# Optimization experiments

Hardware: AMD Instinct MI355X
Metric: run time of the kernel (lower is better)

## Reference

```python
import jax, jax.numpy as jnp
import numpy as np

B, S = 512, 256
NUM_LOC, NUM_USERS, D = 50000, 10000, 256
MAX_RECENT = 5
DQ = D // 4            # user/hour/weekday embed dim
TEMP = 3 * DQ          # temporal feature size
H2 = D // 2            # scorer hidden
NEG = -1e9


def setup_inputs() -> dict:
    key = jax.random.key(0)
    ks = jax.random.split(key, 25)
    p = lambda i, shape: jax.random.normal(ks[i], shape, jnp.float32) * 0.02

    locations = jax.random.randint(ks[0], (B, S), 0, NUM_LOC)
    users = jax.random.randint(ks[1], (B, S), 0, NUM_USERS)
    weekdays = jax.random.randint(ks[2], (B, S), 0, 8)
    start_mins = jax.random.randint(ks[3], (B, S), 0, 1440)
    lengths = jax.random.randint(ks[4], (B,), 1, S + 1)  # ragged valid lengths
    mask = jnp.arange(S)[None, :] < lengths[:, None]     # (B,S) bool prefix mask

    return {
        "locations": locations, "users": users, "weekdays": weekdays,
        "start_mins": start_mins, "mask": mask,
        # embedding tables (padding_idx=0 row zeroed, matching torch init)
        "loc_table": p(5, (NUM_LOC, D)).at[0].set(0.0),
        "user_table": p(6, (NUM_USERS, DQ)).at[0].set(0.0),
        "hour_table": p(7, (25, DQ)).at[0].set(0.0),
        "wd_table": p(8, (8, DQ)).at[0].set(0.0),
        # LSTM (PyTorch layout: gates i,f,g,o stacked)
        "W_ih": p(9, (4 * D, D + TEMP)), "W_hh": p(10, (4 * D, D)),
        "b_ih": p(11, (4 * D,)), "b_hh": p(12, (4 * D,)),
        # recent-location scorer MLP
        "sc_W1": p(13, (H2, D + 2)), "sc_b1": p(14, (H2,)),
        "sc_W2": p(15, (1, H2)), "sc_b2": p(16, (1,)),
        # new-location predictor MLP (dropout is identity in eval)
        "np_W1": p(17, (D, D)), "np_b1": p(18, (D,)),
        "np_W2": p(19, (NUM_LOC, D)), "np_b2": p(20, (NUM_LOC,)),
        # mix predictor
        "mx_W": p(21, (1, D)), "mx_b": p(22, (1,)),
    }


def _forward(locations, users, weekdays, start_mins, mask,
             loc_table, user_table, hour_table, wd_table,
             W_ih, W_hh, b_ih, b_hh,
             sc_W1, sc_b1, sc_W2, sc_b2,
             np_W1, np_b1, np_W2, np_b2, mx_W, mx_b):
    gelu = lambda x: jax.nn.gelu(x, approximate=False)  # torch nn.GELU default

    hours = jnp.clip(start_mins // 60, 0, 24)
    temporal = jnp.concatenate(
        [user_table[users], hour_table[hours], wd_table[weekdays]], axis=-1)
    x = jnp.concatenate([loc_table[locations], temporal], axis=-1)  # (B,S,D+TEMP)

    # --- LSTM over time via scan (PyTorch gate order i,f,g,o) ---
    def step(carry, xt):
        h, c = carry
        g = xt @ W_ih.T + b_ih + h @ W_hh.T + b_hh
        i, f, gg, o = jnp.split(g, 4, axis=-1)
        c = jax.nn.sigmoid(f) * c + jax.nn.sigmoid(i) * jnp.tanh(gg)
        h = jax.nn.sigmoid(o) * jnp.tanh(c)
        return (h, c), h

    h0 = jnp.zeros((x.shape[0], D), x.dtype)
    _, outs = jax.lax.scan(step, (h0, h0), jnp.swapaxes(x, 0, 1))
    output = jnp.swapaxes(outs, 0, 1)  # (B,S,D)

    seq_lens = mask.sum(axis=1).astype(jnp.int32) - 1  # last valid index
    bids = jnp.arange(output.shape[0])
    context = output[bids, seq_lens]                   # (B,D)

    # --- vectorized ragged recent-location scoring (j=0 is last visit) ---
    j = jnp.arange(MAX_RECENT)
    idx = seq_lens[:, None] - j[None, :]               # (B,R) indices from end
    valid = idx >= 0                                   # j < seq_len_b
    idxc = jnp.clip(idx, 0, S - 1)
    bidx = bids[:, None]
    rlocs = locations[bidx, idxc]                      # (B,R)
    rtimes = start_mins[bidx, idxc]
    cur_time = start_mins[bids, seq_lens][:, None]
    tdiff = ((cur_time - rtimes).astype(jnp.float32) / 1440.0)[..., None]
    pos = jnp.broadcast_to(j.astype(jnp.float32), rlocs.shape)[..., None]
    feats = jnp.concatenate([loc_table[rlocs], tdiff, pos], axis=-1)  # (B,R,D+2)
    scores = (gelu(feats @ sc_W1.T + sc_b1) @ sc_W2.T + sc_b2)[..., 0]  # (B,R)

    # drop entry jj if some newer valid entry j' < jj has the same location.
    eq = rlocs[:, :, None] == rlocs[:, None, :]        # (B, jj, j')
    newer = (j[:, None] > j[None, :])[None]            # jj > j'
    dup = jnp.any(eq & newer & valid[:, None, :], axis=-1)
    keep = valid & ~dup
    scatter_locs = jnp.where(keep, rlocs, NUM_LOC)     # out-of-range -> dropped

    recent_logits = jnp.full((rlocs.shape[0], NUM_LOC), NEG, jnp.float32)
    recent_logits = recent_logits.at[bidx, scatter_locs].set(scores, mode='drop')

    new_logits = gelu(context @ np_W1.T + np_b1) @ np_W2.T + np_b2  # (B,NUM_LOC)
    mix = jax.nn.sigmoid(context @ mx_W.T + mx_b) * 0.9 + 0.05     # (B,1)
    return mix * recent_logits + (1.0 - mix) * new_logits


def reference(locations, users, weekdays, start_mins, mask,
              loc_table, user_table, hour_table, wd_table,
              W_ih, W_hh, b_ih, b_hh,
              sc_W1, sc_b1, sc_W2, sc_b2,
              np_W1, np_b1, np_W2, np_b2, mx_W, mx_b):
    return _forward(locations, users, weekdays, start_mins, mask,
                    loc_table, user_table, hour_table, wd_table,
                    W_ih, W_hh, b_ih, b_hh,
                    sc_W1, sc_b1, sc_W2, sc_b2,
                    np_W1, np_b1, np_W2, np_b2, mx_W, mx_b)
```

## Files before the change

### kernel.cpp

```cpp
#include <hip/hip_runtime.h>
#include <hip/hip_bf16.h>
#include <math.h>

#define B_ 512
#define S_ 256
#define D_ 256
#define NLOC 50000
#define KX 448
#define G4 1024
#define NEGV -1000000000.0f

typedef __attribute__((ext_vector_type(8))) short short8;
typedef __attribute__((ext_vector_type(4))) float f32x4;

__device__ __forceinline__ float sigmoidf_(float x){ return 1.0f/(1.0f+expf(-x)); }
__device__ __forceinline__ float geluf_(float x){ return 0.5f*x*(1.0f+erff(x*0.70710678118654752f)); }
__device__ __forceinline__ unsigned short f2bf_(float x){
  __hip_bfloat16 h = __float2bfloat16(x);
  return *(unsigned short*)&h;
}
__device__ __forceinline__ float bf2f_(unsigned short u){
  __hip_bfloat16 h = *(__hip_bfloat16*)&u;
  return __bfloat162float(h);
}
__device__ __forceinline__ float fsig_(float x){
  return __fdividef(1.0f, 1.0f + __expf(-x));
}
__device__ __forceinline__ float ftanh2_(float x){
  float ax = fabsf(x);
  float x2 = x*x;
  float tp = x*(1.0f + x2*(-0.3333333333f + x2*(0.1333333333f + x2*(-0.05396825397f))));
  float e  = __expf(2.0f*fminf(ax, 15.0f));
  float te = 1.0f - __fdividef(2.0f, e + 1.0f);
  te = copysignf(te, x);
  return ax < 0.25f ? tp : te;
}
__device__ __forceinline__ void gld_lds16_(const unsigned short* gsrc, unsigned short* ldst){
  __builtin_amdgcn_global_load_lds((const __attribute__((address_space(1))) void*)gsrc,
                                   (__attribute__((address_space(3))) void*)ldst, 16, 0, 0);
}

__global__ void k_init(int* flag){
  if (blockIdx.x==0 && threadIdx.x==0) *flag = 0;
}

__global__ void k_detect(const unsigned char* m, int* flag){
  int i = blockIdx.x*256 + threadIdx.x;
  if ((i & 1) && i < B_*S_ && m[i]) atomicOr(flag, 1);
}

__global__ void k_seqlen(const void* mp, const int* flag, int* slens){
  int b = blockIdx.x*256 + threadIdx.x;
  if (b >= B_) return;
  int cnt = 0;
  if (*flag){
    const unsigned char* m = (const unsigned char*)mp;
    for (int s=0;s<S_;s++) cnt += (m[b*S_+s] != 0);
  } else {
    const int* m = (const int*)mp;
    for (int s=0;s<S_;s++) cnt += (m[b*S_+s] != 0);
  }
  slens[b] = cnt - 1;
}

__global__ void k_buildw(const float* wih, const float* bih, const float* bhh,
                         unsigned short* Wihbf, float* btot){
  int i = blockIdx.x*256 + threadIdx.x;
  if (i < G4*KX) Wihbf[i] = f2bf_(wih[i]);
  if (i < G4) btot[i] = bih[i] + bhh[i];
}

__global__ void k_packw(const float* __restrict__ whh, unsigned short* __restrict__ Whw){
  int idx = blockIdx.x*256 + threadIdx.x;
  if (idx >= 32768) return;
  int lane = idx & 63, f = (idx>>6)&7, kt = (idx>>9)&7, w = idx>>12;
  int q = f>>1, nt = f&1, l16 = lane&15, quad = lane>>4;
  int row = q*256 + w*32 + nt*16 + l16;
  int col = kt*32 + quad*8;
  const float* s = whh + (size_t)row*256 + col;
  short8 pk;
  #pragma unroll
  for (int e=0;e<8;e++) pk[e] = f2bf_(s[e]);
  *(short8*)(Whw + (size_t)idx*8) = pk;
}

__global__ __launch_bounds__(256) void k_gx(
    const int* __restrict__ loc, const int* __restrict__ usr,
    const int* __restrict__ wdy, const int* __restrict__ sm,
    const float* __restrict__ loct, const float* __restrict__ usert,
    const float* __restrict__ hourt, const float* __restrict__ wdt,
    const unsigned short* __restrict__ Wihbf, const float* __restrict__ btot,
    unsigned short* __restrict__ Gx){
  __shared__ unsigned short As[128][40];
  int tid = threadIdx.x;
  int n0 = blockIdx.x*128, m0 = blockIdx.y*128;
  int w = tid>>6, lane = tid&63;
  int quad = lane>>4, l16 = lane&15;
  int mw = (w>>1)*64, nw = (w&1)*64;
  f32x4 acc[4][4] = {};
  int r0 = tid>>2, seg = tid&3;
  for (int kt=0; kt<14; kt++){
    int k0 = kt*32;
    int kc = k0 + seg*8;
    #pragma unroll
    for (int rr=0; rr<2; rr++){
      int r = r0 + rr*64;
      int row = m0 + r;
      const float* src;
      if (kc < 256)      src = loct  + (size_t)loc[row]*256 + kc;
      else if (kc < 320) src = usert + (size_t)usr[row]*64 + (kc-256);
      else if (kc < 384) { int s = sm[row]; int hh = s/60; if (hh>24) hh=24; if (hh<0) hh=0;
                           src = hourt + (size_t)hh*64 + (kc-320); }
      else               src = wdt   + (size_t)wdy[row]*64 + (kc-384);
      float4 v0 = *(const float4*)(src);
      float4 v1 = *(const float4*)(src+4);
      short8 pk;
      pk[0]=f2bf_(v0.x); pk[1]=f2bf_(v0.y); pk[2]=f2bf_(v0.z); pk[3]=f2bf_(v0.w);
      pk[4]=f2bf_(v1.x); pk[5]=f2bf_(v1.y); pk[6]=f2bf_(v1.z); pk[7]=f2bf_(v1.w);
      *(short8*)&As[r][seg*8] = pk;
    }
    __syncthreads();
    short8 bfrag[4], afrag[4];
    #pragma unroll
    for (int nt=0; nt<4; nt++)
      bfrag[nt] = *(const short8*)(Wihbf + (size_t)(n0+nw+nt*16+l16)*KX + k0 + quad*8);
    #pragma unroll
    for (int mt=0; mt<4; mt++)
      afrag[mt] = *(const short8*)&As[mw+mt*16+l16][quad*8];
    #pragma unroll
    for (int mt=0; mt<4; mt++)
      #pragma unroll
      for (int nt=0; nt<4; nt++)
        acc[mt][nt] = __builtin_amdgcn_mfma_f32_16x16x32_bf16(afrag[mt], bfrag[nt], acc[mt][nt], 0, 0, 0);
    __syncthreads();
  }
  #pragma unroll
  for (int nt=0; nt<4; nt++){
    int col = n0 + nw + nt*16 + l16;
    float bv = btot[col];
    #pragma unroll
    for (int mt=0; mt<4; mt++){
      #pragma unroll
      for (int i=0; i<4; i++){
        int row = m0 + mw + mt*16 + quad*4 + i;
        int bb = row >> 8, tt = row & 255;
        Gx[((size_t)tt*B_ + bb)*G4 + col] = f2bf_(acc[mt][nt][i] + bv);
      }
    }
  }
}

__global__ __launch_bounds__(512, 2) void k_lstm(
    const unsigned short* __restrict__ Gx,
    const unsigned short* __restrict__ Whw,
    float* __restrict__ ctx, const int* __restrict__ slens){
  __shared__ unsigned short h_s[16][256];
  __shared__ unsigned short gx_s[16*1024];
  __shared__ unsigned short whhl[8][8][512];
  __shared__ unsigned short whr[8][4][512];
  int tid = threadIdx.x;
  int w = tid >> 6, lane = tid & 63;
  int quad = lane >> 4, l16 = lane & 15;
  int b0 = blockIdx.x * 16;
  int dw = w * 32;

  for (int i = tid; i < 16*256; i += 512) ((unsigned short*)h_s)[i] = 0;

  #pragma unroll
  for (int c=0; c<8; c++)
    gld_lds16_(Whw + ((size_t)(w*64 + c))*512 + lane*8, &whhl[w][c][0]);

  float cst[2][4] = {{0.f,0.f,0.f,0.f},{0.f,0.f,0.f,0.f}};
  int slq[4];
  #pragma unroll
  for (int i=0;i<4;i++) slq[i] = slens[b0 + quad*4 + i];

  asm volatile("s_waitcnt vmcnt(0) lgkmcnt(0)" ::: "memory");
  __syncthreads();

  const unsigned short* sb = Whw + ((size_t)(w*64 + 8))*512 + lane*8;

  for (int t=0; t<S_; t++){
    {
      const unsigned short* src = Gx + ((size_t)t*B_ + b0)*G4 + w*2048 + lane*8;
      #pragma unroll
      for (int j=0;j<4;j++) gld_lds16_(src + j*512, &gx_s[w*2048 + j*512]);
    }
    #pragma unroll
    for (int j=0;j<3;j++) gld_lds16_(sb + (size_t)j*512, &whr[w][j][0]);
    __builtin_amdgcn_sched_barrier(0);

    short8 af[8];
    #pragma unroll
    for (int kt=0;kt<8;kt++)
      af[kt] = *(const short8*)((const char*)h_s + l16*512 + ((((kt<<2)|quad) ^ (l16&7))<<4));
    f32x4 acc[4][2] = {};
    #pragma unroll
    for (int f=0;f<8;f++)
      acc[f>>1][f&1] = __builtin_amdgcn_mfma_f32_16x16x32_bf16(
          af[0], *(const short8*)&whhl[w][f][lane*8], acc[f>>1][f&1], 0, 0, 0);
    __builtin_amdgcn_sched_barrier(0);

    #pragma unroll
    for (int i=0;i<56;i++){
      if (i+3 < 56) gld_lds16_(sb + (size_t)(i+3)*512, &whr[w][(i+3)&3][0]);
      if (i <= 52)      asm volatile("s_waitcnt vmcnt(3)" ::: "memory");
      else if (i == 53) asm volatile("s_waitcnt vmcnt(2)" ::: "memory");
      else if (i == 54) asm volatile("s_waitcnt vmcnt(1)" ::: "memory");
      else              asm volatile("s_waitcnt vmcnt(0)" ::: "memory");
      __builtin_amdgcn_sched_barrier(0);
      short8 bb = *(const short8*)&whr[w][i&3][lane*8];
      int c = 8+i;
      acc[(c&7)>>1][c&1] = __builtin_amdgcn_mfma_f32_16x16x32_bf16(
          af[c>>3], bb, acc[(c&7)>>1][c&1], 0, 0, 0);
    }

    asm volatile("s_waitcnt vmcnt(0) lgkmcnt(0)" ::: "memory");
    __builtin_amdgcn_sched_barrier(0);
    __builtin_amdgcn_s_barrier();

    const unsigned int* gxw = (const unsigned int*)&gx_s[0];
    int half = l16 & 1;
    #pragma unroll
    for (int nt=0;nt<2;nt++){
      int d = dw + nt*16 + l16;
      int dbase2 = (dw + nt*16) >> 1;
      int chunkx = d >> 3;
      #pragma unroll
      for (int i=0;i<4;i++){
        int r = quad*4 + i;
        int base = r*512 + dbase2 + (l16>>1);
        unsigned int u0 = gxw[base];
        unsigned int u1 = gxw[base + 128];
        unsigned int u2 = gxw[base + 256];
        unsigned int u3 = gxw[base + 384];
        unsigned short s0 = half ? (unsigned short)(u0>>16) : (unsigned short)(u0&0xffff);
        unsigned short s1 = half ? (unsigned short)(u1>>16) : (unsigned short)(u1&0xffff);
        unsigned short s2 = half ? (unsigned short)(u2>>16) : (unsigned short)(u2&0xffff);
        unsigned short s3 = half ? (unsigned short)(u3>>16) : (unsigned short)(u3&0xffff);
        float gi = acc[0][nt][i] + bf2f_(s0);
        float gf = acc[1][nt][i] + bf2f_(s1);
        float gg = acc[2][nt][i] + bf2f_(s2);
        float go = acc[3][nt][i] + bf2f_(s3);
        float cn = fsig_(gf)*cst[nt][i] + fsig_(gi)*ftanh2_(gg);
        float hn = fsig_(go)*ftanh2_(cn);
        cst[nt][i] = cn;
        *(unsigned short*)((char*)h_s + r*512 + ((chunkx ^ (r&7))<<4) + (d&7)*2) = f2bf_(hn);
        if (t == slq[i]) ctx[(size_t)(b0 + r)*D_ + d] = hn;
      }
    }

    asm volatile("s_waitcnt lgkmcnt(0)" ::: "memory");
    __builtin_amdgcn_sched_barrier(0);
    __builtin_amdgcn_s_barrier();
  }
}

__global__ void k_post1(const float* __restrict__ ctx, const float* __restrict__ W1,
                        const float* __restrict__ b1, const float* __restrict__ mxW,
                        const float* __restrict__ mxb, float* newhid, float* mixv){
  __shared__ float cs[256];
  __shared__ float red[256];
  int b = blockIdx.x, tid = threadIdx.x;
  cs[tid] = ctx[(size_t)b*D_ + tid];
  __syncthreads();
  float a = b1[tid];
  const float* wr = W1 + (size_t)tid*D_;
  for (int k=0; k<D_; k++) a += cs[k]*wr[k];
  newhid[(size_t)b*D_ + tid] = geluf_(a);
  red[tid] = cs[tid]*mxW[tid];
  __syncthreads();
  for (int s=128; s>0; s>>=1){ if (tid<s) red[tid]+=red[tid+s]; __syncthreads(); }
  if (tid==0) mixv[b] = sigmoidf_(red[0]+mxb[0])*0.9f + 0.05f;
}

__global__ void k_recent(const int* __restrict__ loc, const int* __restrict__ sm,
                         const int* __restrict__ slens, const float* __restrict__ loct,
                         const float* __restrict__ W1, const float* __restrict__ b1,
                         const float* __restrict__ W2, const float* __restrict__ b2,
                         float* scores, int* rlocs, int* keep){
  __shared__ int rl[5], vs[5];
  __shared__ float td[5];
  __shared__ float red[128];
  int b = blockIdx.x, tid = threadIdx.x;
  int sl = slens[b];
  if (tid < 5){
    int idx = sl - tid;
    int v = idx >= 0;
    int ic = v ? idx : 0;
    rl[tid] = loc[b*S_ + ic];
    vs[tid] = v;
    int cur = sm[b*S_ + sl];
    td[tid] = (float)(cur - sm[b*S_ + ic]) * (1.0f/1440.0f);
  }
  __syncthreads();
  for (int j=0; j<5; j++){
    const float* lrow = loct + (size_t)rl[j]*D_;
    const float* wr = W1 + (size_t)tid*258;
    float a = b1[tid];
    for (int k=0; k<D_; k++) a += lrow[k]*wr[k];
    a += td[j]*wr[256] + (float)j*wr[257];
    red[tid] = geluf_(a)*W2[tid];
    __syncthreads();
    for (int s=64; s>0; s>>=1){ if (tid<s) red[tid]+=red[tid+s]; __syncthreads(); }
    if (tid==0) scores[b*5+j] = red[0] + b2[0];
    __syncthreads();
  }
  if (tid==0){
    for (int j=0; j<5; j++){
      int dup = 0;
      for (int k=0; k<j; k++) dup |= (rl[j]==rl[k]) && vs[k];
      keep[b*5+j] = vs[j] && !dup;
      rlocs[b*5+j] = rl[j];
    }
  }
}

__global__ __launch_bounds__(256) void k_final(const float* __restrict__ newhid,
    const float* __restrict__ W2, const float* __restrict__ b2,
    const float* __restrict__ mixv, float* __restrict__ out){
  __shared__ float Hs[16][260];
  __shared__ float Wl[64][65];
  int tid = threadIdx.x;
  int l0 = blockIdx.x*64, b0 = blockIdx.y*16;
  int ll = tid & 63, bq = tid >> 6;
  #pragma unroll
  for (int r=0; r<16; r++) Hs[r][tid] = newhid[(size_t)(b0+r)*D_ + tid];
  float acc[4] = {0.f,0.f,0.f,0.f};
  for (int kt=0; kt<4; kt++){
    int k0 = kt*64;
    __syncthreads();
    #pragma unroll
    for (int r=0; r<4; r++){
      int row = 4*r + bq;
      int l = l0 + row;
      Wl[row][ll] = (l < NLOC) ? W2[(size_t)l*D_ + k0 + ll] : 0.f;
    }
    __syncthreads();
    #pragma unroll
    for (int kk=0; kk<64; kk++){
      float wv = Wl[ll][kk];
      #pragma unroll
      for (int bi=0; bi<4; bi++) acc[bi] += wv * Hs[bq*4+bi][k0+kk];
    }
  }
  int l = l0 + ll;
  if (l < NLOC){
    float bias = b2[l];
    #pragma unroll
    for (int bi=0; bi<4; bi++){
      int b = b0 + bq*4 + bi;
      float mx = mixv[b];
      out[(size_t)b*NLOC + l] = mx*NEGV + (1.0f-mx)*(acc[bi] + bias);
    }
  }
}

__global__ void k_scatter(const float* __restrict__ newhid, const float* __restrict__ W2,
                          const float* __restrict__ b2, const float* __restrict__ mixv,
                          const float* __restrict__ scores, const int* __restrict__ rlocs,
                          const int* __restrict__ keep, float* out){
  int b = blockIdx.x, lane = threadIdx.x;
  float mx = mixv[b];
  for (int j=0; j<5; j++){
    if (!keep[b*5+j]) continue;
    int rl = rlocs[b*5+j];
    const float* wr = W2 + (size_t)rl*D_;
    const float* hr = newhid + (size_t)b*D_;
    float a = 0.f;
    #pragma unroll
    for (int q=0; q<4; q++){ int k = lane + 64*q; a += hr[k]*wr[k]; }
    #pragma unroll
    for (int off=32; off>0; off>>=1) a += __shfl_xor(a, off, 64);
    if (lane==0)
      out[(size_t)b*NLOC + rl] = mx*scores[b*5+j] + (1.0f-mx)*(a + b2[rl]);
  }
}

extern "C" void kernel_launch(void* const* d_in, const int* in_sizes, int n_in,
                              void* d_out, int out_size, void* d_ws, size_t ws_size,
                              hipStream_t stream){
  const int* locations   = (const int*)d_in[0];
  const int* users       = (const int*)d_in[1];
  const int* weekdays    = (const int*)d_in[2];
  const int* start_mins  = (const int*)d_in[3];
  const void* mask       = d_in[4];
  const float* loc_table = (const float*)d_in[5];
  const float* user_table= (const float*)d_in[6];
  const float* hour_table= (const float*)d_in[7];
  const float* wd_table  = (const float*)d_in[8];
  const float* W_ih      = (const float*)d_in[9];
  const float* W_hh      = (const float*)d_in[10];
  const float* b_ih      = (const float*)d_in[11];
  const float* b_hh      = (const float*)d_in[12];
  const float* sc_W1     = (const float*)d_in[13];
  const float* sc_b1     = (const float*)d_in[14];
  const float* sc_W2     = (const float*)d_in[15];
  const float* sc_b2     = (const float*)d_in[16];
  const float* np_W1     = (const float*)d_in[17];
  const float* np_b1     = (const float*)d_in[18];
  const float* np_W2     = (const float*)d_in[19];
  const float* np_b2     = (const float*)d_in[20];
  const float* mx_W      = (const float*)d_in[21];
  const float* mx_b      = (const float*)d_in[22];
  float* out = (float*)d_out;

  char* w = (char*)d_ws;
  size_t o = 0;
  auto alloc = [&](size_t bytes)->void*{ void* p = w + o; o += (bytes + 255) & ~(size_t)255; return p; };
  unsigned short* Gx    = (unsigned short*)alloc((size_t)B_*S_*G4*sizeof(short));
  unsigned short* Wihbf = (unsigned short*)alloc((size_t)G4*KX*sizeof(short));
  unsigned short* Whw   = (unsigned short*)alloc((size_t)G4*D_*sizeof(short));
  float* btot   = (float*)alloc((size_t)G4*sizeof(float));
  float* ctx    = (float*)alloc((size_t)B_*D_*sizeof(float));
  float* newhid = (float*)alloc((size_t)B_*D_*sizeof(float));
  float* mixv   = (float*)alloc((size_t)B_*sizeof(float));
  float* scores = (float*)alloc((size_t)B_*5*sizeof(float));
  int*   slens  = (int*)alloc((size_t)B_*sizeof(int));
  int*   rlocs  = (int*)alloc((size_t)B_*5*sizeof(int));
  int*   keep   = (int*)alloc((size_t)B_*5*sizeof(int));
  int*   flag   = (int*)alloc(sizeof(int));

  k_init<<<1, 64, 0, stream>>>(flag);
  k_detect<<<512, 256, 0, stream>>>((const unsigned char*)mask, flag);
  k_seqlen<<<2, 256, 0, stream>>>(mask, flag, slens);
  k_buildw<<<1792, 256, 0, stream>>>(W_ih, b_ih, b_hh, Wihbf, btot);
  k_packw<<<128, 256, 0, stream>>>(W_hh, Whw);
  k_gx<<<dim3(8,1024), 256, 0, stream>>>(locations, users, weekdays, start_mins,
                                         loc_table, user_table, hour_table, wd_table,
                                         Wihbf, btot, Gx);
  k_lstm<<<32, 512, 0, stream>>>(Gx, Whw, ctx, slens);
  k_post1<<<512, 256, 0, stream>>>(ctx, np_W1, np_b1, mx_W, mx_b, newhid, mixv);
  k_recent<<<512, 128, 0, stream>>>(locations, start_mins, slens, loc_table,
                                    sc_W1, sc_b1, sc_W2, sc_b2, scores, rlocs, keep);
  k_final<<<dim3(782,32), 256, 0, stream>>>(newhid, np_W2, np_b2, mixv, out);
  k_scatter<<<512, 64, 0, stream>>>(newhid, np_W2, np_b2, mixv, scores, rlocs, keep, out);
}
```

Measured before the change: 3.128 ms.

## Stream W_hh in 4-tile double-buffered groups instead of per-tile ring

The LSTM recurrence kernel now keeps only 4 W_hh tiles resident in LDS per wave instead of 8. The remaining 60 tiles are streamed in groups of 4 through a two-slot double buffer, replacing the 4-deep per-tile ring of 56 tiles. Each group is read from LDS into registers before the next global-to-LDS load overwrites that slot, so each wait covers four MFMAs instead of one. This cuts the number of waitcnt stalls per timestep, at the cost of more streamed traffic per step and the same total LDS use.

```diff
diff --git a/kernel.cpp b/kernel.cpp
--- a/kernel.cpp
+++ b/kernel.cpp
@@ -156,8 +156,8 @@
     float* __restrict__ ctx, const int* __restrict__ slens){
   __shared__ unsigned short h_s[16][256];
   __shared__ unsigned short gx_s[16*1024];
-  __shared__ unsigned short whhl[8][8][512];
-  __shared__ unsigned short whr[8][4][512];
+  __shared__ unsigned short whhl[8][4][512];
+  __shared__ unsigned short whr[8][8][512];
   int tid = threadIdx.x;
   int w = tid >> 6, lane = tid & 63;
   int quad = lane >> 4, l16 = lane & 15;
@@ -167,7 +167,7 @@
   for (int i = tid; i < 16*256; i += 512) ((unsigned short*)h_s)[i] = 0;
 
   #pragma unroll
-  for (int c=0; c<8; c++)
+  for (int c=0; c<4; c++)
     gld_lds16_(Whw + ((size_t)(w*64 + c))*512 + lane*8, &whhl[w][c][0]);
 
   float cst[2][4] = {{0.f,0.f,0.f,0.f},{0.f,0.f,0.f,0.f}};
@@ -178,7 +178,7 @@
   asm volatile("s_waitcnt vmcnt(0) lgkmcnt(0)" ::: "memory");
   __syncthreads();
 
-  const unsigned short* sb = Whw + ((size_t)(w*64 + 8))*512 + lane*8;
+  const unsigned short* sb = Whw + ((size_t)(w*64 + 4))*512 + lane*8;
 
   for (int t=0; t<S_; t++){
     {
@@ -187,7 +187,10 @@
       for (int j=0;j<4;j++) gld_lds16_(src + j*512, &gx_s[w*2048 + j*512]);
     }
     #pragma unroll
-    for (int j=0;j<3;j++) gld_lds16_(sb + (size_t)j*512, &whr[w][j][0]);
+    for (int k=0;k<2;k++)
+      #pragma unroll
+      for (int j=0;j<4;j++)
+        gld_lds16_(sb + (size_t)(4*k+j)*512, &whr[w][k*4+j][0]);
     __builtin_amdgcn_sched_barrier(0);
 
     short8 af[8];
@@ -196,23 +199,33 @@
       af[kt] = *(const short8*)((const char*)h_s + l16*512 + ((((kt<<2)|quad) ^ (l16&7))<<4));
     f32x4 acc[4][2] = {};
     #pragma unroll
-    for (int f=0;f<8;f++)
+    for (int f=0;f<4;f++)
       acc[f>>1][f&1] = __builtin_amdgcn_mfma_f32_16x16x32_bf16(
           af[0], *(const short8*)&whhl[w][f][lane*8], acc[f>>1][f&1], 0, 0, 0);
     __builtin_amdgcn_sched_barrier(0);
 
     #pragma unroll
-    for (int i=0;i<56;i++){
-      if (i+3 < 56) gld_lds16_(sb + (size_t)(i+3)*512, &whr[w][(i+3)&3][0]);
-      if (i <= 52)      asm volatile("s_waitcnt vmcnt(3)" ::: "memory");
-      else if (i == 53) asm volatile("s_waitcnt vmcnt(2)" ::: "memory");
-      else if (i == 54) asm volatile("s_waitcnt vmcnt(1)" ::: "memory");
-      else              asm volatile("s_waitcnt vmcnt(0)" ::: "memory");
+    for (int k=0;k<15;k++){
+      if (k < 14) asm volatile("s_waitcnt vmcnt(4)" ::: "memory");
+      else        asm volatile("s_waitcnt vmcnt(0)" ::: "memory");
       __builtin_amdgcn_sched_barrier(0);
-      short8 bb = *(const short8*)&whr[w][i&3][lane*8];
-      int c = 8+i;
-      acc[(c&7)>>1][c&1] = __builtin_amdgcn_mfma_f32_16x16x32_bf16(
-          af[c>>3], bb, acc[(c&7)>>1][c&1], 0, 0, 0);
+      short8 bb[4];
+      #pragma unroll
+      for (int j=0;j<4;j++) bb[j] = *(const short8*)&whr[w][(k&1)*4+j][lane*8];
+      asm volatile("s_waitcnt lgkmcnt(0)" ::: "memory");
+      __builtin_amdgcn_sched_barrier(0);
+      if (k+2 < 15){
+        #pragma unroll
+        for (int j=0;j<4;j++)
+          gld_lds16_(sb + (size_t)(4*(k+2)+j)*512, &whr[w][(k&1)*4+j][0]);
+      }
+      __builtin_amdgcn_sched_barrier(0);
+      #pragma unroll
+      for (int j=0;j<4;j++){
+        int c = 4 + 4*k + j;
+        acc[(c&7)>>1][c&1] = __builtin_amdgcn_mfma_f32_16x16x32_bf16(
+            af[c>>3], bb[j], acc[(c&7)>>1][c&1], 0, 0, 0);
+      }
     }
 
     asm volatile("s_waitcnt vmcnt(0) lgkmcnt(0)" ::: "memory");
```

After: 3.177 ms. About the same (+1.5%).

## Quantize LSTM recurrent weights and hidden state to FP8 with register-streamed MFMA

Applied to the files above, without the earlier changes.

Recurrent W_hh and the hidden state are packed as FP8 instead of BF16, and the recurrent matmul uses fp8 MFMA. With the smaller footprint, 24 of 64 weight fragments per wave stay in LDS and the rest are streamed from global memory straight into registers in batches of eight, replacing the per-fragment global-to-LDS pipeline and its fine-grained vmcnt waits. This halves weight bandwidth on the serial 256-step recurrence. The cost is that FP8 precision on both weights and h may push accuracy past tolerance.

```diff
diff --git a/kernel.cpp b/kernel.cpp
--- a/kernel.cpp
+++ b/kernel.cpp
@@ -35,7 +35,7 @@
   te = copysignf(te, x);
   return ax < 0.25f ? tp : te;
 }
-__device__ __forceinline__ void gld_lds16_(const unsigned short* gsrc, unsigned short* ldst){
+__device__ __forceinline__ void gld_lds16_(const void* gsrc, void* ldst){
   __builtin_amdgcn_global_load_lds((const __attribute__((address_space(1))) void*)gsrc,
                                    (__attribute__((address_space(3))) void*)ldst, 16, 0, 0);
 }
@@ -70,7 +70,7 @@
   if (i < G4) btot[i] = bih[i] + bhh[i];
 }
 
-__global__ void k_packw(const float* __restrict__ whh, unsigned short* __restrict__ Whw){
+__global__ void k_packw(const float* __restrict__ whh, unsigned char* __restrict__ Ww8){
   int idx = blockIdx.x*256 + threadIdx.x;
   if (idx >= 32768) return;
   int lane = idx & 63, f = (idx>>6)&7, kt = (idx>>9)&7, w = idx>>12;
@@ -78,10 +78,13 @@
   int row = q*256 + w*32 + nt*16 + l16;
   int col = kt*32 + quad*8;
   const float* s = whh + (size_t)row*256 + col;
-  short8 pk;
-  #pragma unroll
-  for (int e=0;e<8;e++) pk[e] = f2bf_(s[e]);
-  *(short8*)(Whw + (size_t)idx*8) = pk;
+  unsigned lo, hi;
+  lo = __builtin_amdgcn_cvt_pk_fp8_f32(s[0], s[1], 0, 0);
+  lo = __builtin_amdgcn_cvt_pk_fp8_f32(s[2], s[3], lo, 1);
+  hi = __builtin_amdgcn_cvt_pk_fp8_f32(s[4], s[5], 0, 0);
+  hi = __builtin_amdgcn_cvt_pk_fp8_f32(s[6], s[7], hi, 1);
+  uint2 v; v.x = lo; v.y = hi;
+  *(uint2*)(Ww8 + (size_t)idx*8) = v;
 }
 
 __global__ __launch_bounds__(256) void k_gx(
@@ -150,25 +153,30 @@
   }
 }
 
+#define CONSUME8(BATCH, CBASE) \
+  _Pragma("unroll") \
+  for (int j=0;j<8;j++){ int c = (CBASE)+j; \
+    acc[(c&7)>>1][c&1] = __builtin_amdgcn_mfma_f32_16x16x32_fp8_fp8( \
+        af[c>>3], BATCH[j], acc[(c&7)>>1][c&1], 0, 0, 0); }
+
 __global__ __launch_bounds__(512, 2) void k_lstm(
     const unsigned short* __restrict__ Gx,
-    const unsigned short* __restrict__ Whw,
+    const unsigned char* __restrict__ Ww8,
     float* __restrict__ ctx, const int* __restrict__ slens){
-  __shared__ unsigned short h_s[16][256];
+  __shared__ unsigned char h_s[16*256];
   __shared__ unsigned short gx_s[16*1024];
-  __shared__ unsigned short whhl[8][8][512];
-  __shared__ unsigned short whr[8][4][512];
+  __shared__ unsigned char whhs[8*12288];
   int tid = threadIdx.x;
   int w = tid >> 6, lane = tid & 63;
   int quad = lane >> 4, l16 = lane & 15;
   int b0 = blockIdx.x * 16;
   int dw = w * 32;
 
-  for (int i = tid; i < 16*256; i += 512) ((unsigned short*)h_s)[i] = 0;
+  for (int i = tid; i < 16*256; i += 512) h_s[i] = 0;
 
   #pragma unroll
-  for (int c=0; c<8; c++)
-    gld_lds16_(Whw + ((size_t)(w*64 + c))*512 + lane*8, &whhl[w][c][0]);
+  for (int j=0;j<12;j++)
+    gld_lds16_(Ww8 + (size_t)w*32768 + j*1024 + lane*16, &whhs[w*12288 + j*1024]);
 
   float cst[2][4] = {{0.f,0.f,0.f,0.f},{0.f,0.f,0.f,0.f}};
   int slq[4];
@@ -178,42 +186,53 @@
   asm volatile("s_waitcnt vmcnt(0) lgkmcnt(0)" ::: "memory");
   __syncthreads();
 
-  const unsigned short* sb = Whw + ((size_t)(w*64 + 8))*512 + lane*8;
-
   for (int t=0; t<S_; t++){
+    unsigned long long pb = (unsigned long long)Ww8;
+    asm volatile("" : "+s"(pb));
+    const unsigned char* sb = (const unsigned char*)pb + (size_t)w*32768 + lane*8;
+
+    long long B1[8], B2[8], B3[8], B4[8], B5[8];
+    #pragma unroll
+    for (int j=0;j<8;j++) B1[j] = *(const long long*)(sb + (size_t)(24+j)*512);
+    #pragma unroll
+    for (int j=0;j<8;j++) B2[j] = *(const long long*)(sb + (size_t)(32+j)*512);
+    __builtin_amdgcn_sched_barrier(0);
+
+    long long af[8];
+    #pragma unroll
+    for (int kt=0;kt<8;kt++)
+      af[kt] = *(const long long*)&h_s[l16*256 + ((((kt<<2)|quad) ^ (l16&7))<<3)];
+    f32x4 acc[4][2] = {};
+    #pragma unroll
+    for (int c=0;c<24;c++){
+      long long bfr = *(const long long*)&whhs[w*12288 + c*512 + lane*8];
+      acc[(c&7)>>1][c&1] = __builtin_amdgcn_mfma_f32_16x16x32_fp8_fp8(
+          af[c>>3], bfr, acc[(c&7)>>1][c&1], 0, 0, 0);
+    }
+    __builtin_amdgcn_sched_barrier(0);
+
+    #pragma unroll
+    for (int j=0;j<8;j++) B3[j] = *(const long long*)(sb + (size_t)(40+j)*512);
     {
       const unsigned short* src = Gx + ((size_t)t*B_ + b0)*G4 + w*2048 + lane*8;
       #pragma unroll
       for (int j=0;j<4;j++) gld_lds16_(src + j*512, &gx_s[w*2048 + j*512]);
     }
-    #pragma unroll
-    for (int j=0;j<3;j++) gld_lds16_(sb + (size_t)j*512, &whr[w][j][0]);
-    __builtin_amdgcn_sched_barrier(0);
-
-    short8 af[8];
-    #pragma unroll
-    for (int kt=0;kt<8;kt++)
-      af[kt] = *(const short8*)((const char*)h_s + l16*512 + ((((kt<<2)|quad) ^ (l16&7))<<4));
-    f32x4 acc[4][2] = {};
-    #pragma unroll
-    for (int f=0;f<8;f++)
-      acc[f>>1][f&1] = __builtin_amdgcn_mfma_f32_16x16x32_bf16(
-          af[0], *(const short8*)&whhl[w][f][lane*8], acc[f>>1][f&1], 0, 0, 0);
-    __builtin_amdgcn_sched_barrier(0);
-
-    #pragma unroll
-    for (int i=0;i<56;i++){
-      if (i+3 < 56) gld_lds16_(sb + (size_t)(i+3)*512, &whr[w][(i+3)&3][0]);
-      if (i <= 52)      asm volatile("s_waitcnt vmcnt(3)" ::: "memory");
-      else if (i == 53) asm volatile("s_waitcnt vmcnt(2)" ::: "memory");
-      else if (i == 54) asm volatile("s_waitcnt vmcnt(1)" ::: "memory");
-      else              asm volatile("s_waitcnt vmcnt(0)" ::: "memory");
-      __builtin_amdgcn_sched_barrier(0);
-      short8 bb = *(const short8*)&whr[w][i&3][lane*8];
-      int c = 8+i;
-      acc[(c&7)>>1][c&1] = __builtin_amdgcn_mfma_f32_16x16x32_bf16(
-          af[c>>3], bb, acc[(c&7)>>1][c&1], 0, 0, 0);
-    }
+    __builtin_amdgcn_sched_barrier(0);
+
+    CONSUME8(B1, 24)
+    #pragma unroll
+    for (int j=0;j<8;j++) B4[j] = *(const long long*)(sb + (size_t)(48+j)*512);
+    __builtin_amdgcn_sched_barrier(0);
+
+    CONSUME8(B2, 32)
+    #pragma unroll
+    for (int j=0;j<8;j++) B5[j] = *(const long long*)(sb + (size_t)(56+j)*512);
+    __builtin_amdgcn_sched_barrier(0);
+
+    CONSUME8(B3, 40)
+    CONSUME8(B4, 48)
+    CONSUME8(B5, 56)
 
     asm volatile("s_waitcnt vmcnt(0) lgkmcnt(0)" ::: "memory");
     __builtin_amdgcn_sched_barrier(0);
@@ -225,7 +244,6 @@
     for (int nt=0;nt<2;nt++){
       int d = dw + nt*16 + l16;
       int dbase2 = (dw + nt*16) >> 1;
-      int chunkx = d >> 3;
       #pragma unroll
       for (int i=0;i<4;i++){
         int r = quad*4 + i;
@@ -245,7 +263,8 @@
         float cn = fsig_(gf)*cst[nt][i] + fsig_(gi)*ftanh2_(gg);
         float hn = fsig_(go)*ftanh2_(cn);
         cst[nt][i] = cn;
-        *(unsigned short*)((char*)h_s + r*512 + ((chunkx ^ (r&7))<<4) + (d&7)*2) = f2bf_(hn);
+        int p8 = __builtin_amdgcn_cvt_pk_fp8_f32(hn, hn, 0, 0);
+        h_s[r*256 + (((d>>3) ^ (r&7))<<3) + (d&7)] = (unsigned char)(p8 & 0xff);
         if (t == slq[i]) ctx[(size_t)(b0 + r)*D_ + d] = hn;
       }
     }
@@ -410,7 +429,7 @@
   auto alloc = [&](size_t bytes)->void*{ void* p = w + o; o += (bytes + 255) & ~(size_t)255; return p; };
   unsigned short* Gx    = (unsigned short*)alloc((size_t)B_*S_*G4*sizeof(short));
   unsigned short* Wihbf = (unsigned short*)alloc((size_t)G4*KX*sizeof(short));
-  unsigned short* Whw   = (unsigned short*)alloc((size_t)G4*D_*sizeof(short));
+  unsigned char*  Ww8   = (unsigned char*)alloc((size_t)G4*D_);
   float* btot   = (float*)alloc((size_t)G4*sizeof(float));
   float* ctx    = (float*)alloc((size_t)B_*D_*sizeof(float));
   float* newhid = (float*)alloc((size_t)B_*D_*sizeof(float));
@@ -425,11 +444,11 @@
   k_detect<<<512, 256, 0, stream>>>((const unsigned char*)mask, flag);
   k_seqlen<<<2, 256, 0, stream>>>(mask, flag, slens);
   k_buildw<<<1792, 256, 0, stream>>>(W_ih, b_ih, b_hh, Wihbf, btot);
-  k_packw<<<128, 256, 0, stream>>>(W_hh, Whw);
+  k_packw<<<128, 256, 0, stream>>>(W_hh, Ww8);
   k_gx<<<dim3(8,1024), 256, 0, stream>>>(locations, users, weekdays, start_mins,
                                          loc_table, user_table, hour_table, wd_table,
                                          Wihbf, btot, Gx);
-  k_lstm<<<32, 512, 0, stream>>>(Gx, Whw, ctx, slens);
+  k_lstm<<<32, 512, 0, stream>>>(Gx, Ww8, ctx, slens);
   k_post1<<<512, 256, 0, stream>>>(ctx, np_W1, np_b1, mx_W, mx_b, newhid, mixv);
   k_recent<<<512, 128, 0, stream>>>(locations, start_mins, slens, loc_table,
                                     sc_W1, sc_b1, sc_W2, sc_b2, scores, rlocs, keep);
```

Result: faster. 2.982 ms (-4.7%).
